# Kernel tuning notes

Measured on AMD Instinct MI355X. Metric: run time of the kernel, lower is better.

Reference implementation:

```python
import jax, jax.numpy as jnp
import numpy as np

KEY_DIM = 32
D = 128  # attn_ratio * key_dim
H = 8
DIM = 512
N = 1024
B = 16
EPS = 1e-5


def setup_inputs() -> dict:
    key = jax.random.key(0)
    ks = jax.random.split(key, 5)
    x = jax.random.normal(ks[0], (B, DIM, N), dtype=jnp.float32)
    # grouped Conv1d(dim -> H*(2*key_dim+d), k=1, groups=H): per-group weight [H, 192, 64]
    qkv_w = jax.random.normal(ks[1], (H, 2 * KEY_DIM + D, DIM // H), dtype=jnp.float32) * 0.05
    qkv_b = jax.random.normal(ks[2], (H, 2 * KEY_DIM + D), dtype=jnp.float32) * 0.02
    # proj Conv1d(d*H -> dim, k=1)
    proj_w = jax.random.normal(ks[3], (DIM, D * H), dtype=jnp.float32) * 0.03
    proj_b = jax.random.normal(ks[4], (DIM,), dtype=jnp.float32) * 0.02
    bn_gamma = jnp.ones((DIM,), dtype=jnp.float32)
    bn_beta = jnp.zeros((DIM,), dtype=jnp.float32)
    bn_mean = jnp.zeros((DIM,), dtype=jnp.float32)
    bn_var = jnp.ones((DIM,), dtype=jnp.float32)
    return {"x": x, "qkv_w": qkv_w, "qkv_b": qkv_b, "proj_w": proj_w,
            "proj_b": proj_b, "bn_gamma": bn_gamma, "bn_beta": bn_beta,
            "bn_mean": bn_mean, "bn_var": bn_var}


def reference(x, qkv_w, qkv_b, proj_w, proj_b, bn_gamma, bn_beta, bn_mean, bn_var):
    Bx, C, Nx = x.shape
    scale = KEY_DIM ** (-0.5)
    # grouped 1x1 conv: split channels into H groups of C//H
    xh = x.reshape(Bx, H, C // H, Nx)                      # [B,H,Cg,N]
    qkv = jnp.einsum('bhcn,hoc->bhon', xh, qkv_w) + qkv_b[None, :, :, None]
    q, k, v = jnp.split(qkv, [KEY_DIM, 2 * KEY_DIM], axis=2)  # [B,H,kd,N],[B,H,kd,N],[B,H,d,N]
    # attn[m,n] = sum_c q[c,m]*k[c,n]
    attn = jnp.einsum('bhcm,bhcn->bhmn', q, k) * scale      # [B,H,N,N]
    attn = jax.nn.softmax(attn, axis=-1)
    # out[d,m] = sum_n v[d,n]*attn[m,n]  (v @ attn^T)
    o = jnp.einsum('bhdn,bhmn->bhdm', v, attn)              # [B,H,d,N]
    o = o.reshape(Bx, H * D, Nx)
    # proj: ReLU -> 1x1 conv -> BatchNorm1d (inference mode)
    o = jax.nn.relu(o)
    o = jnp.einsum('bcn,oc->bon', o, proj_w) + proj_b[None, :, None]
    inv = bn_gamma / jnp.sqrt(bn_var + EPS)
    o = o * inv[None, :, None] + (bn_beta - bn_mean * inv)[None, :, None]
    return o
```

## Files before the change

kernel.cpp:

```cpp
#include <hip/hip_runtime.h>
#include <math.h>

typedef unsigned short u16;
typedef unsigned int u32;

#define Bb   16
#define Hh   8
#define KD   32
#define DV   128
#define DIM  512
#define Nn   1024
#define OQKV 192
#define SCALE2 0.25503490221320355f

typedef short bf16x8 __attribute__((ext_vector_type(8)));
typedef float f32x16 __attribute__((ext_vector_type(16)));

#define MFMA32(a, b, c) __builtin_amdgcn_mfma_f32_32x32x16_bf16(a, b, c, 0, 0, 0)

__device__ __forceinline__ float fexp2(float x) {
#if __has_builtin(__builtin_amdgcn_exp2f)
  return __builtin_amdgcn_exp2f(x);
#else
  return exp2f(x);
#endif
}

__device__ __forceinline__ u16 f2bf_rn(float f) {
  return (u16)((__float_as_uint(f) + 0x8000u) >> 16);
}

#if __has_builtin(__builtin_amdgcn_cvt_pk_bf16_f32)
__device__ __forceinline__ u32 pk2(float lo, float hi) {
  auto r = __builtin_amdgcn_cvt_pk_bf16_f32(lo, hi);
  return __builtin_bit_cast(u32, r);
}
#else
__device__ __forceinline__ u32 pk2(float lo, float hi) {
  u32 a = __float_as_uint(lo) + 0x8000u;
  u32 b = __float_as_uint(hi) + 0x8000u;
  return __builtin_amdgcn_perm(b, a, 0x07060302);
}
#endif

#if __has_builtin(__builtin_amdgcn_permlane32_swap)
__device__ __forceinline__ void pswap(u32& a, u32& b) {
  auto r = __builtin_amdgcn_permlane32_swap(a, b, false, false);
  a = r[0]; b = r[1];
}
#else
__device__ __forceinline__ void pswap(u32& a, u32& b) {
  asm("v_permlane32_swap_b32 %0, %1" : "+v"(a), "+v"(b));
}
#endif

__device__ __forceinline__ uint4 cvt8(const float* __restrict__ src) {
  float4 a = *(const float4*)src;
  float4 b = *(const float4*)(src + 4);
  uint4 r;
  r.x = pk2(a.x, a.y); r.y = pk2(a.z, a.w);
  r.z = pk2(b.x, b.y); r.w = pk2(b.z, b.w);
  return r;
}

__global__ __launch_bounds__(256) void qkv_kernel(
    const float* __restrict__ x, const float* __restrict__ qw,
    const float* __restrict__ bias, u16* __restrict__ Qb,
    u16* __restrict__ Kb, u16* __restrict__ Vb) {
  const int nt = blockIdx.x, bh = blockIdx.y;
  const int b = bh >> 3, h = bh & 7;
  const int tid = threadIdx.x;
  const int wid = tid >> 6, lane = tid & 63;
  const int r32 = lane & 31, hh = lane >> 5;
  const int n0 = nt * 128;

  __shared__ __align__(16) union SH {
    struct { u16 Ws[192 * 72]; u16 Xs[128 * 72]; } s;
    struct { u16 Vt[128 * 136]; u16 Qs[128 * 32]; u16 Ks[128 * 32]; } o;
  } sh;

  const float* wqp = qw + (size_t)h * OQKV * 64;
  #pragma unroll
  for (int i = 0; i < 6; ++i) {
    int idx = i * 256 + tid;
    int o = idx >> 3, c8 = (idx & 7) * 8;
    *(uint4*)&sh.s.Ws[o * 72 + c8] = cvt8(&wqp[o * 64 + c8]);
  }
  const float* xp = x + ((size_t)b * DIM + h * 64) * Nn + n0;
  #pragma unroll
  for (int i = 0; i < 4; ++i) {
    int idx = i * 256 + tid;
    int cp = idx >> 5, n4 = (idx & 31) * 4;
    const int c = 2 * cp;
    float4 a = *(const float4*)&xp[(size_t)c * Nn + n4];
    float4 d = *(const float4*)&xp[(size_t)(c + 1) * Nn + n4];
    *(u32*)&sh.s.Xs[(n4 + 0) * 72 + c] = pk2(a.x, d.x);
    *(u32*)&sh.s.Xs[(n4 + 1) * 72 + c] = pk2(a.y, d.y);
    *(u32*)&sh.s.Xs[(n4 + 2) * 72 + c] = pk2(a.z, d.z);
    *(u32*)&sh.s.Xs[(n4 + 3) * 72 + c] = pk2(a.w, d.w);
  }
  __syncthreads();

  f32x16 acc[6];
  #pragma unroll
  for (int t = 0; t < 6; ++t)
    #pragma unroll
    for (int r = 0; r < 16; ++r) acc[t][r] = 0.0f;

  const int nw = wid * 32;
  #pragma unroll
  for (int k = 0; k < 4; ++k) {
    const int ko = k * 16 + hh * 8;
    bf16x8 xb = *(const bf16x8*)&sh.s.Xs[(nw + r32) * 72 + ko];
    #pragma unroll
    for (int t = 0; t < 6; ++t) {
      bf16x8 wa = *(const bf16x8*)&sh.s.Ws[(t * 32 + r32) * 72 + ko];
      acc[t] = MFMA32(wa, xb, acc[t]);
    }
  }

  __syncthreads();

  const int nl = nw + r32;
  const float* bp = bias + h * OQKV;
  #pragma unroll
  for (int t = 0; t < 6; ++t) {
    #pragma unroll
    for (int g = 0; g < 4; ++g) {
      const int ob = t * 32 + 8 * g + 4 * hh;
      float4 bv = *(const float4*)&bp[ob];
      float v0 = acc[t][4 * g + 0] + bv.x;
      float v1 = acc[t][4 * g + 1] + bv.y;
      float v2 = acc[t][4 * g + 2] + bv.z;
      float v3 = acc[t][4 * g + 3] + bv.w;
      if (t == 0) {
        uint2 pk;
        pk.x = pk2(v0 * SCALE2, v1 * SCALE2);
        pk.y = pk2(v2 * SCALE2, v3 * SCALE2);
        *(uint2*)&sh.o.Qs[nl * 32 + ob] = pk;
      } else if (t == 1) {
        uint2 pk; pk.x = pk2(v0, v1); pk.y = pk2(v2, v3);
        *(uint2*)&sh.o.Ks[nl * 32 + ob - 32] = pk;
      } else {
        const int d = ob - 64;
        sh.o.Vt[(d + 0) * 136 + nl] = f2bf_rn(v0);
        sh.o.Vt[(d + 1) * 136 + nl] = f2bf_rn(v1);
        sh.o.Vt[(d + 2) * 136 + nl] = f2bf_rn(v2);
        sh.o.Vt[(d + 3) * 136 + nl] = f2bf_rn(v3);
      }
    }
  }
  __syncthreads();

  const int dd0 = tid >> 4;
  const int nn = (tid & 15) * 8;
  #pragma unroll
  for (int i = 0; i < 8; ++i) {
    const int dd = dd0 + i * 16;
    uint4 vv = *(const uint4*)&sh.o.Vt[dd * 136 + nn];
    *(uint4*)&Vb[((size_t)bh * DV + dd) * Nn + n0 + nn] = vv;
  }
  {
    const size_t base = ((size_t)bh * Nn + n0) * 32;
    uint4 q0 = *(const uint4*)&sh.o.Qs[tid * 16];
    uint4 q1 = *(const uint4*)&sh.o.Qs[tid * 16 + 8];
    *(uint4*)&Qb[base + tid * 16] = q0;
    *(uint4*)&Qb[base + tid * 16 + 8] = q1;
    uint4 k0 = *(const uint4*)&sh.o.Ks[tid * 16];
    uint4 k1 = *(const uint4*)&sh.o.Ks[tid * 16 + 8];
    *(uint4*)&Kb[base + tid * 16] = k0;
    *(uint4*)&Kb[base + tid * 16 + 8] = k1;
  }
}

__global__ __launch_bounds__(256) void attn_kernel(
    const u16* __restrict__ Qb, const u16* __restrict__ Kb,
    const u16* __restrict__ Vb, u16* __restrict__ Ot) {
  const int blk = blockIdx.x;
  const int xcd = blk & 7, j = blk >> 3;
  const int bh = (xcd << 4) | (j >> 3);
  const int mt = j & 7;
  const int tid = threadIdx.x;
  const int wid = tid >> 6, lane = tid & 63;
  const int r32 = lane & 31, hh = lane >> 5;
  const int mw = mt * 128 + wid * 32;

  __shared__ __align__(16) u16 Vs[2][128 * 72];

  const u16* qp = Qb + ((size_t)bh * Nn + mw + r32) * 32;
  const bf16x8 qb0 = *(const bf16x8*)&qp[hh * 8];
  const bf16x8 qb1 = *(const bf16x8*)&qp[16 + hh * 8];

  const u16* kbase = Kb + (size_t)bh * Nn * 32;
  const u16* vbase = Vb + (size_t)bh * DV * Nn;

  int sd[4], sn[4];
  #pragma unroll
  for (int i = 0; i < 4; ++i) {
    int idx = i * 256 + tid;
    sd[i] = idx >> 3; sn[i] = (idx & 7) * 8;
  }

  uint4 vreg[4];
  #pragma unroll
  for (int i = 0; i < 4; ++i)
    vreg[i] = *(const uint4*)&vbase[(size_t)sd[i] * Nn + sn[i]];
  #pragma unroll
  for (int i = 0; i < 4; ++i)
    *(uint4*)&Vs[0][sd[i] * 72 + sn[i]] = vreg[i];

  bf16x8 ka[4];
  {
    const u16* kp0 = kbase + (size_t)r32 * 32;
    const u16* kp1 = kbase + (size_t)(32 + r32) * 32;
    ka[0] = *(const bf16x8*)&kp0[hh * 8];
    ka[1] = *(const bf16x8*)&kp0[16 + hh * 8];
    ka[2] = *(const bf16x8*)&kp1[hh * 8];
    ka[3] = *(const bf16x8*)&kp1[16 + hh * 8];
  }
  f32x16 c0, c1;
  #pragma unroll
  for (int r = 0; r < 16; ++r) { c0[r] = 0.0f; c1[r] = 0.0f; }
  c0 = MFMA32(ka[0], qb0, c0);
  c0 = MFMA32(ka[1], qb1, c0);
  c1 = MFMA32(ka[2], qb0, c1);
  c1 = MFMA32(ka[3], qb1, c1);

  {
    const u16* kp0 = kbase + (size_t)(64 + r32) * 32;
    const u16* kp1 = kbase + (size_t)(96 + r32) * 32;
    ka[0] = *(const bf16x8*)&kp0[hh * 8];
    ka[1] = *(const bf16x8*)&kp0[16 + hh * 8];
    ka[2] = *(const bf16x8*)&kp1[hh * 8];
    ka[3] = *(const bf16x8*)&kp1[16 + hh * 8];
  }

  f32x16 o[4];
  #pragma unroll
  for (int t = 0; t < 4; ++t)
    #pragma unroll
    for (int r = 0; r < 16; ++r) o[t][r] = 0.0f;
  float lsum = 0.0f;
  u32 Pk[16];
  union { u32 d[4]; bf16x8 v; } pbf[4];

  auto finishS = [&]() {
    float csum = 0.0f;
    #pragma unroll
    for (int r = 0; r < 16; ++r) { c0[r] = fexp2(c0[r]); csum += c0[r]; }
    #pragma unroll
    for (int r = 0; r < 16; ++r) { c1[r] = fexp2(c1[r]); csum += c1[r]; }
    lsum += csum;
    #pragma unroll
    for (int g = 0; g < 4; ++g) {
      Pk[2 * g]     = pk2(c0[4 * g + 0], c0[4 * g + 1]);
      Pk[2 * g + 1] = pk2(c0[4 * g + 2], c0[4 * g + 3]);
      Pk[8 + 2 * g]     = pk2(c1[4 * g + 0], c1[4 * g + 1]);
      Pk[8 + 2 * g + 1] = pk2(c1[4 * g + 2], c1[4 * g + 3]);
    }
    pswap(Pk[0], Pk[2]);   pswap(Pk[1], Pk[3]);
    pswap(Pk[4], Pk[6]);   pswap(Pk[5], Pk[7]);
    pswap(Pk[8], Pk[10]);  pswap(Pk[9], Pk[11]);
    pswap(Pk[12], Pk[14]); pswap(Pk[13], Pk[15]);
    #pragma unroll
    for (int i = 0; i < 4; ++i) {
      pbf[i].d[0] = Pk[4 * i + 0];
      pbf[i].d[1] = Pk[4 * i + 1];
      pbf[i].d[2] = Pk[4 * i + 2];
      pbf[i].d[3] = Pk[4 * i + 3];
    }
  };

  finishS();

  for (int ch = 0; ch < 15; ++ch) {
    const int p = ch & 1;
    __syncthreads();

    #pragma unroll
    for (int i = 0; i < 4; ++i)
      vreg[i] = *(const uint4*)&vbase[(size_t)sd[i] * Nn + (ch + 1) * 64 + sn[i]];

    __builtin_amdgcn_s_setprio(1);
    #pragma unroll
    for (int r = 0; r < 16; ++r) { c0[r] = 0.0f; c1[r] = 0.0f; }
    c0 = MFMA32(ka[0], qb0, c0);
    c0 = MFMA32(ka[1], qb1, c0);
    c1 = MFMA32(ka[2], qb0, c1);
    c1 = MFMA32(ka[3], qb1, c1);

    bf16x8 kn[4];
    {
      const u16* kp0 = kbase + (size_t)((ch + 2) * 64 + r32) * 32;
      const u16* kp1 = kbase + (size_t)((ch + 2) * 64 + 32 + r32) * 32;
      kn[0] = *(const bf16x8*)&kp0[hh * 8];
      kn[1] = *(const bf16x8*)&kp0[16 + hh * 8];
      kn[2] = *(const bf16x8*)&kp1[hh * 8];
      kn[3] = *(const bf16x8*)&kp1[16 + hh * 8];
    }

    #pragma unroll
    for (int t = 0; t < 4; ++t) {
      const u16* vrow = &Vs[p][(t * 32 + r32) * 72];
      #pragma unroll
      for (int s = 0; s < 4; ++s) {
        bf16x8 va = *(const bf16x8*)&vrow[s * 16 + hh * 8];
        o[t] = MFMA32(va, pbf[s].v, o[t]);
      }
    }
    __builtin_amdgcn_s_setprio(0);

    #pragma unroll
    for (int i = 0; i < 4; ++i)
      *(uint4*)&Vs[1 - p][sd[i] * 72 + sn[i]] = vreg[i];

    finishS();

    #pragma unroll
    for (int i = 0; i < 4; ++i) ka[i] = kn[i];
  }

  __syncthreads();
  __builtin_amdgcn_s_setprio(1);
  #pragma unroll
  for (int t = 0; t < 4; ++t) {
    const u16* vrow = &Vs[1][(t * 32 + r32) * 72];
    #pragma unroll
    for (int s = 0; s < 4; ++s) {
      bf16x8 va = *(const bf16x8*)&vrow[s * 16 + hh * 8];
      o[t] = MFMA32(va, pbf[s].v, o[t]);
    }
  }
  __builtin_amdgcn_s_setprio(0);

  lsum += __shfl_xor(lsum, 32, 64);
  const float inv = 1.0f / lsum;
  const int m = mw + r32;
  const int b = bh >> 3, h = bh & 7;
  u16* obase = Ot + ((size_t)b * Nn + m) * 1024 + h * DV + 4 * hh;
  #pragma unroll
  for (int t = 0; t < 4; ++t) {
    #pragma unroll
    for (int g = 0; g < 4; ++g) {
      float v0 = fmaxf(o[t][4 * g + 0] * inv, 0.0f);
      float v1 = fmaxf(o[t][4 * g + 1] * inv, 0.0f);
      float v2 = fmaxf(o[t][4 * g + 2] * inv, 0.0f);
      float v3 = fmaxf(o[t][4 * g + 3] * inv, 0.0f);
      uint2 pk; pk.x = pk2(v0, v1); pk.y = pk2(v2, v3);
      *(uint2*)&obase[t * 32 + 8 * g] = pk;
    }
  }
}

__global__ __launch_bounds__(256) void proj_kernel(
    const u16* __restrict__ Ot, const float* __restrict__ pw,
    const float* __restrict__ pb, const float* __restrict__ g,
    const float* __restrict__ bt, const float* __restrict__ mn,
    const float* __restrict__ vr, float* __restrict__ out) {
  const int blk = blockIdx.x;
  const int xcd = blk & 7, rr = blk >> 3;
  const int pairl = rr >> 2, oct = rr & 3;
  const int pair = xcd * 16 + pairl;
  const int b = pair >> 3, nt = pair & 7;
  const int n0 = nt * 128, oc0 = oct * 128;
  const int tid = threadIdx.x;
  const int wid = tid >> 6, lane = tid & 63;
  const int r32 = lane & 31, hh = lane >> 5;
  const int ocw = (wid >> 1) * 64, nw = (wid & 1) * 64;

  __shared__ __align__(16) u16 Ws[128 * 72];
  __shared__ __align__(16) u16 Os[128 * 72];
  __shared__ __align__(16) float invL[128];
  __shared__ __align__(16) float addL[128];

  if (tid < 128) {
    const int oc = oc0 + tid;
    float inv = g[oc] * rsqrtf(vr[oc] + 1e-5f);
    invL[tid] = inv;
    addL[tid] = pb[oc] * inv + bt[oc] - mn[oc] * inv;
  }

  f32x16 o[2][2];
  #pragma unroll
  for (int t = 0; t < 2; ++t)
    #pragma unroll
    for (int u = 0; u < 2; ++u)
      #pragma unroll
      for (int r = 0; r < 16; ++r) o[t][u][r] = 0.0f;

  for (int ic0 = 0; ic0 < 1024; ic0 += 64) {
    __syncthreads();
    #pragma unroll
    for (int i = 0; i < 4; ++i) {
      int idx = i * 256 + tid;
      int row = idx >> 3, c8 = (idx & 7) * 8;
      *(uint4*)&Ws[row * 72 + c8] =
          cvt8(&pw[(size_t)(oc0 + row) * 1024 + ic0 + c8]);
    }
    #pragma unroll
    for (int i = 0; i < 4; ++i) {
      int idx = i * 256 + tid;
      int row = idx >> 3, c8 = (idx & 7) * 8;
      *(uint4*)&Os[row * 72 + c8] =
          *(const uint4*)&Ot[((size_t)b * Nn + n0 + row) * 1024 + ic0 + c8];
    }
    __syncthreads();

    #pragma unroll
    for (int s = 0; s < 4; ++s) {
      const int ko = s * 16 + hh * 8;
      bf16x8 a0 = *(const bf16x8*)&Ws[(ocw + r32) * 72 + ko];
      bf16x8 a1 = *(const bf16x8*)&Ws[(ocw + 32 + r32) * 72 + ko];
      bf16x8 b0 = *(const bf16x8*)&Os[(nw + r32) * 72 + ko];
      bf16x8 b1 = *(const bf16x8*)&Os[(nw + 32 + r32) * 72 + ko];
      o[0][0] = MFMA32(a0, b0, o[0][0]);
      o[0][1] = MFMA32(a0, b1, o[0][1]);
      o[1][0] = MFMA32(a1, b0, o[1][0]);
      o[1][1] = MFMA32(a1, b1, o[1][1]);
    }
  }

  #pragma unroll
  for (int t = 0; t < 2; ++t) {
    const int lbase = ocw + t * 32 + 4 * hh;
    #pragma unroll
    for (int g = 0; g < 4; ++g) {
      const int l = lbase + 8 * g;
      const int oc = oc0 + l;
      float4 iv = *(const float4*)&invL[l];
      float4 av = *(const float4*)&addL[l];
      #pragma unroll
      for (int u = 0; u < 2; ++u) {
        const int n = n0 + nw + u * 32 + r32;
        out[((size_t)b * DIM + oc + 0) * Nn + n] = o[t][u][4 * g + 0] * iv.x + av.x;
        out[((size_t)b * DIM + oc + 1) * Nn + n] = o[t][u][4 * g + 1] * iv.y + av.y;
        out[((size_t)b * DIM + oc + 2) * Nn + n] = o[t][u][4 * g + 2] * iv.z + av.z;
        out[((size_t)b * DIM + oc + 3) * Nn + n] = o[t][u][4 * g + 3] * iv.w + av.w;
      }
    }
  }
}

extern "C" void kernel_launch(void* const* d_in, const int* in_sizes, int n_in,
                              void* d_out, int out_size, void* d_ws,
                              size_t ws_size, hipStream_t stream) {
  const float* x      = (const float*)d_in[0];
  const float* qkv_w  = (const float*)d_in[1];
  const float* qkv_b  = (const float*)d_in[2];
  const float* proj_w = (const float*)d_in[3];
  const float* proj_b = (const float*)d_in[4];
  const float* bn_g   = (const float*)d_in[5];
  const float* bn_b   = (const float*)d_in[6];
  const float* bn_m   = (const float*)d_in[7];
  const float* bn_v   = (const float*)d_in[8];
  float* out = (float*)d_out;

  char* ws = (char*)d_ws;
  u16* Qb   = (u16*)(ws);
  u16* Kb   = (u16*)(ws + 8388608);
  u16* Vb   = (u16*)(ws + 16777216);
  u16* Ot   = (u16*)(ws + 50331648);

  qkv_kernel<<<dim3(8, Bb * Hh), 256, 0, stream>>>(x, qkv_w, qkv_b, Qb, Kb, Vb);
  attn_kernel<<<dim3(1024), 256, 0, stream>>>(Qb, Kb, Vb, Ot);
  proj_kernel<<<dim3(512), 256, 0, stream>>>(Ot, proj_w, proj_b, bn_g, bn_b,
                                             bn_m, bn_v, out);
}
```

Baseline: 189.1 us.

## Unroll attention loop by two, split exp-sum chains, widen proj K-tile

The attention main loop is unrolled by two with a macro, and the two K register sets ping-pong between steps, which removes the per-iteration register copy and the dynamic LDS buffer index. The row-sum of exponentials now uses four independent accumulators instead of one serial chain. In the projection kernel the reduction tile grows from 64 to 128 input channels. That halves the number of barrier pairs but doubles LDS use per block, which may reduce occupancy.

After: 214.8 us. 1.14x slower.

```diff
diff --git a/kernel.cpp b/kernel.cpp
--- a/kernel.cpp
+++ b/kernel.cpp
@@ -209,7 +209,7 @@
   for (int i = 0; i < 4; ++i)
     *(uint4*)&Vs[0][sd[i] * 72 + sn[i]] = vreg[i];
 
-  bf16x8 ka[4];
+  bf16x8 ka[4], kb[4];
   {
     const u16* kp0 = kbase + (size_t)r32 * 32;
     const u16* kp1 = kbase + (size_t)(32 + r32) * 32;
@@ -245,12 +245,22 @@
   union { u32 d[4]; bf16x8 v; } pbf[4];
 
   auto finishS = [&]() {
-    float csum = 0.0f;
-    #pragma unroll
-    for (int r = 0; r < 16; ++r) { c0[r] = fexp2(c0[r]); csum += c0[r]; }
-    #pragma unroll
-    for (int r = 0; r < 16; ++r) { c1[r] = fexp2(c1[r]); csum += c1[r]; }
-    lsum += csum;
+    #pragma unroll
+    for (int r = 0; r < 16; ++r) c0[r] = fexp2(c0[r]);
+    #pragma unroll
+    for (int r = 0; r < 16; ++r) c1[r] = fexp2(c1[r]);
+    float t0 = 0.0f, t1 = 0.0f, t2 = 0.0f, t3 = 0.0f;
+    #pragma unroll
+    for (int r = 0; r < 4; ++r) {
+      t0 += c0[r];      t1 += c0[4 + r];
+      t2 += c0[8 + r];  t3 += c0[12 + r];
+    }
+    #pragma unroll
+    for (int r = 0; r < 4; ++r) {
+      t0 += c1[r];      t1 += c1[4 + r];
+      t2 += c1[8 + r];  t3 += c1[12 + r];
+    }
+    lsum += (t0 + t1) + (t2 + t3);
     #pragma unroll
     for (int g = 0; g < 4; ++g) {
       Pk[2 * g]     = pk2(c0[4 * g + 0], c0[4 * g + 1]);
@@ -273,52 +283,51 @@
 
   finishS();
 
-  for (int ch = 0; ch < 15; ++ch) {
-    const int p = ch & 1;
-    __syncthreads();
-
-    #pragma unroll
-    for (int i = 0; i < 4; ++i)
-      vreg[i] = *(const uint4*)&vbase[(size_t)sd[i] * Nn + (ch + 1) * 64 + sn[i]];
-
-    __builtin_amdgcn_s_setprio(1);
-    #pragma unroll
-    for (int r = 0; r < 16; ++r) { c0[r] = 0.0f; c1[r] = 0.0f; }
-    c0 = MFMA32(ka[0], qb0, c0);
-    c0 = MFMA32(ka[1], qb1, c0);
-    c1 = MFMA32(ka[2], qb0, c1);
-    c1 = MFMA32(ka[3], qb1, c1);
-
-    bf16x8 kn[4];
-    {
-      const u16* kp0 = kbase + (size_t)((ch + 2) * 64 + r32) * 32;
-      const u16* kp1 = kbase + (size_t)((ch + 2) * 64 + 32 + r32) * 32;
-      kn[0] = *(const bf16x8*)&kp0[hh * 8];
-      kn[1] = *(const bf16x8*)&kp0[16 + hh * 8];
-      kn[2] = *(const bf16x8*)&kp1[hh * 8];
-      kn[3] = *(const bf16x8*)&kp1[16 + hh * 8];
-    }
-
-    #pragma unroll
-    for (int t = 0; t < 4; ++t) {
-      const u16* vrow = &Vs[p][(t * 32 + r32) * 72];
-      #pragma unroll
-      for (int s = 0; s < 4; ++s) {
-        bf16x8 va = *(const bf16x8*)&vrow[s * 16 + hh * 8];
-        o[t] = MFMA32(va, pbf[s].v, o[t]);
-      }
-    }
-    __builtin_amdgcn_s_setprio(0);
-
-    #pragma unroll
-    for (int i = 0; i < 4; ++i)
-      *(uint4*)&Vs[1 - p][sd[i] * 72 + sn[i]] = vreg[i];
-
-    finishS();
-
-    #pragma unroll
-    for (int i = 0; i < 4; ++i) ka[i] = kn[i];
-  }
+#define ATTN_STEP(CH, P, KIN, KOUT)                                            \
+  {                                                                            \
+    __syncthreads();                                                           \
+    _Pragma("unroll")                                                          \
+    for (int i = 0; i < 4; ++i)                                                \
+      vreg[i] =                                                                \
+          *(const uint4*)&vbase[(size_t)sd[i] * Nn + ((CH) + 1) * 64 + sn[i]]; \
+    __builtin_amdgcn_s_setprio(1);                                             \
+    _Pragma("unroll")                                                          \
+    for (int r = 0; r < 16; ++r) { c0[r] = 0.0f; c1[r] = 0.0f; }               \
+    c0 = MFMA32(KIN[0], qb0, c0);                                              \
+    c0 = MFMA32(KIN[1], qb1, c0);                                              \
+    c1 = MFMA32(KIN[2], qb0, c1);                                              \
+    c1 = MFMA32(KIN[3], qb1, c1);                                              \
+    {                                                                          \
+      const u16* kp0 = kbase + (size_t)(((CH) + 2) * 64 + r32) * 32;           \
+      const u16* kp1 = kbase + (size_t)(((CH) + 2) * 64 + 32 + r32) * 32;      \
+      KOUT[0] = *(const bf16x8*)&kp0[hh * 8];                                  \
+      KOUT[1] = *(const bf16x8*)&kp0[16 + hh * 8];                             \
+      KOUT[2] = *(const bf16x8*)&kp1[hh * 8];                                  \
+      KOUT[3] = *(const bf16x8*)&kp1[16 + hh * 8];                             \
+    }                                                                          \
+    _Pragma("unroll")                                                          \
+    for (int t = 0; t < 4; ++t) {                                              \
+      const u16* vrow = &Vs[P][(t * 32 + r32) * 72];                           \
+      _Pragma("unroll")                                                        \
+      for (int s = 0; s < 4; ++s) {                                            \
+        bf16x8 va = *(const bf16x8*)&vrow[s * 16 + hh * 8];                    \
+        o[t] = MFMA32(va, pbf[s].v, o[t]);                                     \
+      }                                                                        \
+    }                                                                          \
+    __builtin_amdgcn_s_setprio(0);                                             \
+    _Pragma("unroll")                                                          \
+    for (int i = 0; i < 4; ++i)                                                \
+      *(uint4*)&Vs[(P) ^ 1][sd[i] * 72 + sn[i]] = vreg[i];                     \
+    finishS();                                                                 \
+  }
+
+  for (int pr = 0; pr < 7; ++pr) {
+    const int ch = 2 * pr;
+    ATTN_STEP(ch, 0, ka, kb);
+    ATTN_STEP(ch + 1, 1, kb, ka);
+  }
+  ATTN_STEP(14, 0, ka, kb);
+#undef ATTN_STEP
 
   __syncthreads();
   __builtin_amdgcn_s_setprio(1);
@@ -368,8 +377,8 @@
   const int r32 = lane & 31, hh = lane >> 5;
   const int ocw = (wid >> 1) * 64, nw = (wid & 1) * 64;
 
-  __shared__ __align__(16) u16 Ws[128 * 72];
-  __shared__ __align__(16) u16 Os[128 * 72];
+  __shared__ __align__(16) u16 Ws[128 * 136];
+  __shared__ __align__(16) u16 Os[128 * 136];
   __shared__ __align__(16) float invL[128];
   __shared__ __align__(16) float addL[128];
 
@@ -388,31 +397,31 @@
       #pragma unroll
       for (int r = 0; r < 16; ++r) o[t][u][r] = 0.0f;
 
-  for (int ic0 = 0; ic0 < 1024; ic0 += 64) {
+  for (int ic0 = 0; ic0 < 1024; ic0 += 128) {
     __syncthreads();
     #pragma unroll
-    for (int i = 0; i < 4; ++i) {
+    for (int i = 0; i < 8; ++i) {
       int idx = i * 256 + tid;
-      int row = idx >> 3, c8 = (idx & 7) * 8;
-      *(uint4*)&Ws[row * 72 + c8] =
+      int row = idx >> 4, c8 = (idx & 15) * 8;
+      *(uint4*)&Ws[row * 136 + c8] =
           cvt8(&pw[(size_t)(oc0 + row) * 1024 + ic0 + c8]);
     }
     #pragma unroll
-    for (int i = 0; i < 4; ++i) {
+    for (int i = 0; i < 8; ++i) {
       int idx = i * 256 + tid;
-      int row = idx >> 3, c8 = (idx & 7) * 8;
-      *(uint4*)&Os[row * 72 + c8] =
+      int row = idx >> 4, c8 = (idx & 15) * 8;
+      *(uint4*)&Os[row * 136 + c8] =
           *(const uint4*)&Ot[((size_t)b * Nn + n0 + row) * 1024 + ic0 + c8];
     }
     __syncthreads();
 
     #pragma unroll
-    for (int s = 0; s < 4; ++s) {
+    for (int s = 0; s < 8; ++s) {
       const int ko = s * 16 + hh * 8;
-      bf16x8 a0 = *(const bf16x8*)&Ws[(ocw + r32) * 72 + ko];
-      bf16x8 a1 = *(const bf16x8*)&Ws[(ocw + 32 + r32) * 72 + ko];
-      bf16x8 b0 = *(const bf16x8*)&Os[(nw + r32) * 72 + ko];
-      bf16x8 b1 = *(const bf16x8*)&Os[(nw + 32 + r32) * 72 + ko];
+      bf16x8 a0 = *(const bf16x8*)&Ws[(ocw + r32) * 136 + ko];
+      bf16x8 a1 = *(const bf16x8*)&Ws[(ocw + 32 + r32) * 136 + ko];
+      bf16x8 b0 = *(const bf16x8*)&Os[(nw + r32) * 136 + ko];
+      bf16x8 b1 = *(const bf16x8*)&Os[(nw + 32 + r32) * 136 + ko];
       o[0][0] = MFMA32(a0, b0, o[0][0]);
       o[0][1] = MFMA32(a0, b1, o[0][1]);
       o[1][0] = MFMA32(a1, b0, o[1][0]);
```
